# Kernel optimization log

Hardware: AMD Instinct MI355X
Metric: run time of the kernel (lower is better)

## Reference

```python
import jax, jax.numpy as jnp
import numpy as np


def _compute_gradient(f, src, dst, egw):
    # f: [b, c, n] node features; src/dst: [b, e] edge endpoints; egw: [b, e, d]
    # gradient at node src = sum_edges pinvdx * (f[dst] - f[src])
    fT = f.transpose(0, 2, 1)  # b, n, c
    n = fT.shape[1]
    f_dst = jnp.take_along_axis(fT, dst[..., None], axis=1)  # b, e, c
    f_src = jnp.take_along_axis(fT, src[..., None], axis=1)  # b, e, c
    msg = egw[..., :, None] * (f_dst - f_src)[..., None, :]  # b, e, d, c
    b, e, d, c = msg.shape

    def seg(m, s):
        return jax.ops.segment_sum(m.reshape(e, d * c), s, num_segments=n)

    grad = jax.vmap(seg)(msg, src)  # b, n, d*c
    return grad.transpose(0, 2, 1)  # b, d*c, n


def _forward(x, t, nodes, node_weights, edge_gradient_weights, modes, sp_L,
             fc0_w, fc0_b, Wc, Ws, W0, ws_w, ws_b, gws_w, gws_b,
             fc1_w, fc1_b, fc2_w, fc2_b, directed_edges):
    D = nodes.shape[-1]
    # Fourier bases: modes [k,d,w] scaled by sp_L [d,w]
    temp = jnp.einsum('bxd,kdw->bxkw', nodes, modes * sp_L)
    bc, bs = jnp.cos(temp), jnp.sin(temp)
    b0 = jnp.ones(temp[:, :, :1, :].shape, temp.dtype)
    nw = node_weights[:, :, None, :]
    wbc, wbs, wb0 = bc * nw, bs * nw, b0 * nw

    x_value = x[:, :, :D]
    h = jnp.concatenate([x, t], -1) @ fc0_w + fc0_b  # b, n, c
    h = h.transpose(0, 2, 1)  # b, c, n

    src = directed_edges[..., 0]
    dst = directed_edges[..., 1]
    nlayers = ws_w.shape[0]
    for i in range(nlayers):
        # spectral convolution (real Fourier transform on scattered points)
        xc = jnp.einsum('bcx,bxkw->bckw', h, wbc)
        xs = -jnp.einsum('bcx,bxkw->bckw', h, wbs)
        x0 = jnp.einsum('bcx,bxkw->bckw', h, wb0)
        fc_ = jnp.einsum('bikw,iokw->bokw', xc, Wc[i]) - jnp.einsum('bikw,iokw->bokw', xs, Ws[i])
        fs_ = jnp.einsum('bikw,iokw->bokw', xs, Wc[i]) + jnp.einsum('bikw,iokw->bokw', xc, Ws[i])
        f0_ = jnp.einsum('bikw,iokw->bokw', x0, W0[i])
        x1 = (jnp.einsum('bokw,bxkw->box', f0_, b0)
              + 2.0 * jnp.einsum('bokw,bxkw->box', fc_, bc)
              - 2.0 * jnp.einsum('bokw,bxkw->box', fs_, bs))
        # pointwise linear (Conv1d kernel size 1)
        x2 = jnp.einsum('oc,bcx->box', ws_w[i], h) + ws_b[i][None, :, None]
        # gradient operator + softsign + Conv1d
        g = _compute_gradient(h, src, dst, edge_gradient_weights)  # b, d*c, n
        g = g / (1.0 + jnp.abs(g))  # softsign
        x3 = jnp.einsum('oc,bcx->box', gws_w[i], g) + gws_b[i][None, :, None]
        h = x1 + x2 + x3
        if i != nlayers - 1:
            h = jax.nn.gelu(h, approximate=False)

    h = h.transpose(0, 2, 1)  # b, n, c
    h = jax.nn.gelu(h @ fc1_w + fc1_b, approximate=False)
    h = h @ fc2_w + fc2_b
    return x_value + t * h


def setup_inputs() -> dict:
    B, N, E = 2, 20000, 100000
    D, W, K, C, L, FC, OUT = 3, 1, 128, 128, 3, 128, 3
    key = jax.random.key(0)
    k = jax.random.split(key, 16)
    x = jax.random.normal(k[0], (B, N, D), jnp.float32)
    t = jax.random.uniform(k[1], (B, N, 1), jnp.float32)
    node_mask = jnp.ones((B, N, 1), jnp.int32)
    nodes = jax.random.uniform(k[2], (B, N, D), jnp.float32)
    node_weights = jax.random.uniform(k[3], (B, N, W), jnp.float32) / N
    directed_edges = jax.random.randint(k[4], (B, E, 2), 0, N)
    edge_gradient_weights = jax.random.normal(k[5], (B, E, D), jnp.float32)
    modes = jax.random.normal(k[6], (K, D, W), jnp.float32) * (2.0 * np.pi)
    sp_L = jnp.ones((D, W), jnp.float32)
    fc0_w = jax.random.normal(k[7], (D + 1, C), jnp.float32) * 0.1
    fc0_b = jnp.zeros((C,), jnp.float32)
    scale = 1.0 / (C * C)
    Wc = jax.random.uniform(k[8], (L, C, C, K, W), jnp.float32) * scale
    Ws = jax.random.uniform(k[9], (L, C, C, K, W), jnp.float32) * scale
    W0 = jax.random.uniform(k[10], (L, C, C, 1, W), jnp.float32) * scale
    ws_w = jax.random.normal(k[11], (L, C, C), jnp.float32) * 0.05
    ws_b = jnp.zeros((L, C), jnp.float32)
    gws_w = jax.random.normal(k[12], (L, C, D * C), jnp.float32) * 0.05
    gws_b = jnp.zeros((L, C), jnp.float32)
    fc1_w = jax.random.normal(k[13], (C, FC), jnp.float32) * 0.05
    fc1_b = jnp.zeros((FC,), jnp.float32)
    fc2_w = jax.random.normal(k[14], (FC, OUT), jnp.float32) * 0.05
    fc2_b = jnp.zeros((OUT,), jnp.float32)
    return dict(x=x, t=t, node_mask=node_mask, nodes=nodes, node_weights=node_weights,
                directed_edges=directed_edges, edge_gradient_weights=edge_gradient_weights,
                modes=modes, sp_L=sp_L, fc0_w=fc0_w, fc0_b=fc0_b, Wc=Wc, Ws=Ws, W0=W0,
                ws_w=ws_w, ws_b=ws_b, gws_w=gws_w, gws_b=gws_b,
                fc1_w=fc1_w, fc1_b=fc1_b, fc2_w=fc2_w, fc2_b=fc2_b)


def reference(x, t, node_mask, nodes, node_weights, directed_edges, edge_gradient_weights,
              modes, sp_L, fc0_w, fc0_b, Wc, Ws, W0, ws_w, ws_b, gws_w, gws_b,
              fc1_w, fc1_b, fc2_w, fc2_b):
    del node_mask  # unpacked but unused in the original forward
    return _forward(x, t, nodes, node_weights, edge_gradient_weights, modes, sp_L,
                    fc0_w, fc0_b, Wc, Ws, W0, ws_w, ws_b, gws_w, gws_b,
                    fc1_w, fc1_b, fc2_w, fc2_b, directed_edges)
```

## Files before the change

### kernel.cpp

```cpp
#include <hip/hip_runtime.h>
#include <math.h>

#define BB 2
#define NN 20000
#define EE 100000
#define DD 3
#define KK 128
#define CC 128
#define LL 3
#define FCC 128
#define GJ (DD*CC)
#define KR 768
#define NP 20096
#define NCHK 157
#define G1CH 157
#define G1N 128

typedef __attribute__((ext_vector_type(8))) short bf16x8;
typedef __attribute__((ext_vector_type(4))) float f32x4;

__device__ inline unsigned short f2bf(float f) {
  unsigned int u = __float_as_uint(f);
  u += 0x7fffu + ((u >> 16) & 1u);
  return (unsigned short)(u >> 16);
}
__device__ inline float bf2f(unsigned short u) {
  return __uint_as_float(((unsigned int)u) << 16);
}

__device__ float d_nw[BB*NN];
__device__ __align__(16) unsigned short d_stackT[(size_t)BB*NP*KR];
__device__ __align__(16) unsigned short d_bcT[(size_t)BB*KK*NP];
__device__ __align__(16) unsigned short d_bsT[(size_t)BB*KK*NP];
__device__ __align__(16) unsigned short d_hTwT[(size_t)BB*CC*NP];
__device__ __align__(16) float d_uT[(size_t)BB*NP*FCC];
__device__ __align__(16) unsigned short d_Amatb[BB*CC*KR];
__device__ __align__(16) unsigned short d_fc1wb[FCC*CC];
__device__ __align__(16) float d_part[(size_t)BB*G1CH*2*128*128];
__device__ float d_xc[BB*CC*KK];
__device__ float d_xs[BB*CC*KK];
__device__ float d_x0p[BB*NCHK*CC];
__device__ float d_fcp[BB*CC*8*KK];
__device__ float d_fsp[BB*CC*8*KK];
__device__ float d_bias[BB*CC];
__device__ int d_cnt[BB*NN];
__device__ int d_cursor[BB*NN];
__device__ int d_off[BB*(NN+1)];
__device__ __align__(16) float4 d_erec[(size_t)BB*EE];

__global__ __launch_bounds__(128) void k_basis(const float* __restrict__ nodes,
                                               const float* __restrict__ nodew,
                                               const float* __restrict__ modes,
                                               const float* __restrict__ spL) {
  int bn = blockIdx.x;
  int k  = threadIdx.x;
  int b = bn / NN, n = bn % NN;
  float x0 = nodes[bn*3+0], x1 = nodes[bn*3+1], x2 = nodes[bn*3+2];
  float tmp = x0*modes[k*3+0]*spL[0] + x1*modes[k*3+1]*spL[1] + x2*modes[k*3+2]*spL[2];
  float cv = cosf(tmp), sv = sinf(tmp);
  size_t row = (size_t)(b*NP + n);
  d_stackT[row*KR + k]       = f2bf(cv);
  d_stackT[row*KR + 128 + k] = f2bf(sv);
  if (k == 0) d_nw[bn] = nodew[bn];
}

__global__ __launch_bounds__(256) void k_basisT() {
  __shared__ unsigned short t1[32][136];
  __shared__ unsigned short t2[32][136];
  int blk = blockIdx.x;
  int nt = blk % 628, b = blk / 628;
  int n0 = nt*32;
  int tid = threadIdx.x;
  int kl = tid & 127, ng = tid >> 7;
  for (int nn = ng; nn < 32; nn += 2) {
    int n = n0 + nn;
    unsigned short cv = 0, sv = 0;
    if (n < NN) {
      const unsigned short* sp = d_stackT + ((size_t)(b*NP + n))*KR;
      cv = sp[kl]; sv = sp[128 + kl];
    }
    t1[nn][kl] = cv;
    t2[nn][kl] = sv;
  }
  __syncthreads();
  int nl = tid & 31, kg = tid >> 5;
  for (int k = kg; k < 128; k += 8) {
    d_bcT[((size_t)(b*KK + k))*NP + n0 + nl] = t1[nl][k];
    d_bsT[((size_t)(b*KK + k))*NP + n0 + nl] = t2[nl][k];
  }
}

__global__ __launch_bounds__(256) void k_csr_zero() {
  int tid = blockIdx.x*256 + threadIdx.x;
  if (tid < BB*NN) { d_cnt[tid] = 0; d_cursor[tid] = 0; }
}

__global__ __launch_bounds__(256) void k_csr_count(const int* __restrict__ edges) {
  int e = blockIdx.x*256 + threadIdx.x;
  if (e >= BB*EE) return;
  int b = e / EE;
  int src = edges[e*2 + 0];
  atomicAdd(&d_cnt[b*NN + src], 1);
}

__global__ __launch_bounds__(1024) void k_csr_scan() {
  int b = blockIdx.x;
  __shared__ int sdata[1024];
  __shared__ int carry_s;
  int tid = threadIdx.x;
  if (tid == 0) carry_s = 0;
  __syncthreads();
  for (int chunk = 0; chunk < 20; ++chunk) {
    int i = chunk*1024 + tid;
    int v = (i < NN) ? d_cnt[b*NN + i] : 0;
    sdata[tid] = v;
    __syncthreads();
    for (int s = 1; s < 1024; s <<= 1) {
      int tv = (tid >= s) ? sdata[tid - s] : 0;
      __syncthreads();
      sdata[tid] += tv;
      __syncthreads();
    }
    int excl = carry_s + sdata[tid] - v;
    if (i < NN) d_off[b*(NN+1) + i] = excl;
    __syncthreads();
    if (tid == 1023) carry_s += sdata[1023];
    __syncthreads();
  }
  if (tid == 0) d_off[b*(NN+1) + NN] = carry_s;
}

__global__ __launch_bounds__(256) void k_csr_scatter(const int* __restrict__ edges,
                                                     const float* __restrict__ egw) {
  int e = blockIdx.x*256 + threadIdx.x;
  if (e >= BB*EE) return;
  int b = e / EE;
  int src = edges[e*2 + 0];
  int dst = edges[e*2 + 1];
  int pos = atomicAdd(&d_cursor[b*NN + src], 1);
  d_erec[(size_t)b*EE + d_off[b*(NN+1) + src] + pos] =
      make_float4(__int_as_float(dst), egw[e*3+0], egw[e*3+1], egw[e*3+2]);
}

__global__ __launch_bounds__(256) void k_h0(const float* __restrict__ x,
                                            const float* __restrict__ t,
                                            const float* __restrict__ w,
                                            const float* __restrict__ bias) {
  int tid = blockIdx.x*256 + threadIdx.x;
  int c = tid & 127;
  int bn = tid >> 7;
  int b = bn / NN, n = bn % NN;
  const float* xv = x + bn*3;
  float acc = bias[c] + xv[0]*w[c] + xv[1]*w[CC+c] + xv[2]*w[2*CC+c]
            + t[bn]*w[3*CC+c];
  d_stackT[((size_t)(b*NP + n))*KR + 256 + c] = f2bf(acc);
}

__global__ __launch_bounds__(256) void k_hT0() {
  __shared__ unsigned short t[128][136];
  int chunk = blockIdx.x;
  int b = blockIdx.y;
  int n0 = chunk*128;
  int tid = threadIdx.x;
  int cl = tid & 127, ng = tid >> 7;
  for (int nn = ng; nn < 128; nn += 2) {
    int n = n0 + nn;
    unsigned short v = 0;
    if (n < NN) {
      float hv = bf2f(d_stackT[((size_t)(b*NP + n))*KR + 256 + cl]);
      v = f2bf(hv * d_nw[b*NN + n]);
    }
    t[nn][cl] = v;
  }
  __syncthreads();
  int nl = tid & 31, cg = tid >> 5;
  for (int c = cg; c < 128; c += 8)
    for (int nn2 = 0; nn2 < 128; nn2 += 32)
      d_hTwT[((size_t)(b*CC + c))*NP + n0 + nn2 + nl] = t[nn2 + nl][c];
}

__global__ __launch_bounds__(256) void k_gemm1m() {
  __shared__ unsigned short Bsh[2][128][40];
  int chunk = blockIdx.x;
  int b = blockIdx.y;
  int tid = threadIdx.x, lane = tid & 63, wid = tid >> 6;
  int q = lane >> 4, m = lane & 15;
  f32x4 accC[2][8], accS[2][8];
  #pragma unroll
  for (int i = 0; i < 2; i++)
    #pragma unroll
    for (int j = 0; j < 8; j++) { accC[i][j] = (f32x4){0.f,0.f,0.f,0.f}; accS[i][j] = (f32x4){0.f,0.f,0.f,0.f}; }
  const unsigned short* Ab = d_hTwT + (size_t)b*CC*NP;
  const unsigned short* Bcp = d_bcT + (size_t)b*KK*NP;
  const unsigned short* Bsp = d_bsT + (size_t)b*KK*NP;
  int n0 = chunk*G1N;
  for (int s = 0; s < G1N/32; s++) {
    int nb = n0 + s*32;
    __syncthreads();
    {
      int arr = tid >> 7, row = tid & 127;
      const unsigned short* src = (arr ? Bsp : Bcp) + (size_t)row*NP + nb;
      unsigned short* dr = &Bsh[arr][row][0];
      *(uint4*)&dr[0]  = *(const uint4*)&src[0];
      *(uint4*)&dr[8]  = *(const uint4*)&src[8];
      *(uint4*)&dr[16] = *(const uint4*)&src[16];
      *(uint4*)&dr[24] = *(const uint4*)&src[24];
    }
    __syncthreads();
    bf16x8 a0 = *(const bf16x8*)(Ab + (size_t)(wid*32 + m)*NP + nb + q*8);
    bf16x8 a1 = *(const bf16x8*)(Ab + (size_t)(wid*32 + 16 + m)*NP + nb + q*8);
    #pragma unroll
    for (int kt = 0; kt < 8; kt++) {
      bf16x8 bcf = *(const bf16x8*)&Bsh[0][kt*16 + m][q*8];
      bf16x8 bsf = *(const bf16x8*)&Bsh[1][kt*16 + m][q*8];
      accC[0][kt] = __builtin_amdgcn_mfma_f32_16x16x32_bf16(a0, bcf, accC[0][kt], 0, 0, 0);
      accC[1][kt] = __builtin_amdgcn_mfma_f32_16x16x32_bf16(a1, bcf, accC[1][kt], 0, 0, 0);
      accS[0][kt] = __builtin_amdgcn_mfma_f32_16x16x32_bf16(a0, bsf, accS[0][kt], 0, 0, 0);
      accS[1][kt] = __builtin_amdgcn_mfma_f32_16x16x32_bf16(a1, bsf, accS[1][kt], 0, 0, 0);
    }
  }
  float* base = d_part + (((size_t)b*G1CH + chunk)*2)*16384;
  #pragma unroll
  for (int mt = 0; mt < 2; mt++)
    #pragma unroll
    for (int kt = 0; kt < 8; kt++)
      #pragma unroll
      for (int r = 0; r < 4; r++) {
        int c = wid*32 + mt*16 + q*4 + r;
        int k = kt*16 + m;
        base[c*128 + k]         =  accC[mt][kt][r];
        base[16384 + c*128 + k] = -accS[mt][kt][r];
      }
}

__global__ __launch_bounds__(256) void k_reduce1() {
  int tid = blockIdx.x*256 + threadIdx.x;
  int k = tid & 127;
  int c = (tid >> 7) & 127;
  int arr = (tid >> 14) & 1;
  int b = tid >> 15;
  const float* p = d_part + (((size_t)b*G1CH)*2 + arr)*16384 + c*128 + k;
  float acc = 0.f;
  for (int ch = 0; ch < G1CH; ch++) acc += p[(size_t)ch*2*16384];
  if (arr == 0) d_xc[(b*CC + c)*KK + k] = acc;
  else          d_xs[(b*CC + c)*KK + k] = acc;
}

__global__ __launch_bounds__(256) void k_x0() {
  int chunk = blockIdx.x;
  int b = blockIdx.y;
  int tid = threadIdx.x;
  int c = tid >> 1, half = tid & 1;
  const unsigned short* p = d_hTwT + ((size_t)(b*CC + c))*NP + chunk*128 + half*64;
  float acc = 0.f;
  #pragma unroll
  for (int i = 0; i < 8; i++) {
    ushort4 v0 = *(const ushort4*)&p[i*8];
    ushort4 v1 = *(const ushort4*)&p[i*8 + 4];
    acc += bf2f(v0.x) + bf2f(v0.y) + bf2f(v0.z) + bf2f(v0.w)
         + bf2f(v1.x) + bf2f(v1.y) + bf2f(v1.z) + bf2f(v1.w);
  }
  __shared__ float red[128][2];
  red[c][half] = acc;
  __syncthreads();
  if (half == 0) d_x0p[(b*NCHK + chunk)*CC + c] = red[c][0] + red[c][1];
}

__global__ __launch_bounds__(128) void k_spec(const float* __restrict__ Wc,
                                              const float* __restrict__ Ws, int l) {
  int bo = blockIdx.x;
  int ch = blockIdx.y;
  int b = bo >> 7;
  int o = bo & 127;
  int k = threadIdx.x;
  int i0 = ch*16;
  const float* wcp = Wc + ((size_t)(l*CC + i0)*CC + o)*KK + k;
  const float* wsp = Ws + ((size_t)(l*CC + i0)*CC + o)*KK + k;
  float fc = 0.f, fs = 0.f;
  #pragma unroll 4
  for (int j = 0; j < 16; j++) {
    int i = i0 + j;
    float xcv = d_xc[(b*CC + i)*KK + k];
    float xsv = d_xs[(b*CC + i)*KK + k];
    float wcv = wcp[(size_t)j*CC*KK];
    float wsv = wsp[(size_t)j*CC*KK];
    fc += xcv*wcv - xsv*wsv;
    fs += xsv*wcv + xcv*wsv;
  }
  d_fcp[((size_t)bo*8 + ch)*KK + k] = fc;
  d_fsp[((size_t)bo*8 + ch)*KK + k] = fs;
}

__global__ __launch_bounds__(128) void k_f0(const float* __restrict__ W0,
                                            const float* __restrict__ wsb,
                                            const float* __restrict__ gwsb, int l) {
  int b = blockIdx.x;
  int o = threadIdx.x;
  __shared__ float sx[CC];
  float xv = 0.f;
  for (int p = 0; p < NCHK; p++) xv += d_x0p[(b*NCHK + p)*CC + o];
  sx[o] = xv;
  __syncthreads();
  float acc = 0.f;
  for (int i = 0; i < CC; i++) acc += sx[i]*W0[(l*CC + i)*CC + o];
  d_bias[b*CC + o] = acc + wsb[l*CC + o] + gwsb[l*CC + o];
}

__global__ __launch_bounds__(128) void k_buildAb(const float* __restrict__ wsw,
                                                 const float* __restrict__ gwsw, int l) {
  int bo = blockIdx.x;
  int b = bo >> 7, o = bo & 127;
  int t = threadIdx.x;
  float fc = 0.f, fs = 0.f;
  #pragma unroll
  for (int ch = 0; ch < 8; ch++) {
    fc += d_fcp[((size_t)bo*8 + ch)*KK + t];
    fs += d_fsp[((size_t)bo*8 + ch)*KK + t];
  }
  unsigned short* dst = d_Amatb + (size_t)bo*KR;
  dst[t]       = f2bf( 2.f*fc);
  dst[128 + t] = f2bf(-2.f*fs);
  dst[256 + t] = f2bf(wsw[(l*CC + o)*CC + t]);
  #pragma unroll
  for (int j = 0; j < 3; j++)
    dst[384 + j*128 + t] = f2bf(gwsw[(size_t)(l*CC + o)*GJ + j*128 + t]);
}

__global__ __launch_bounds__(128) void k_fc1w(const float* __restrict__ fc1w) {
  int c = blockIdx.x;
  int o2 = threadIdx.x;
  d_fc1wb[o2*CC + c] = f2bf(fc1w[c*FCC + o2]);
}

__global__ __launch_bounds__(128) void k_grad_csr() {
  int bn = blockIdx.x;
  int b = bn / NN, n = bn % NN;
  int c = threadIdx.x;
  int beg = d_off[b*(NN+1) + n];
  int end = d_off[b*(NN+1) + n + 1];
  const float4* rp = d_erec + (size_t)b*EE;
  const unsigned short* hb = d_stackT + (size_t)b*NP*KR + 256 + c;
  float a0 = 0.f, a1 = 0.f, a2 = 0.f;
  float sw0 = 0.f, sw1 = 0.f, sw2 = 0.f;
  int p = beg;
  for (; p + 4 <= end; p += 4) {
    float4 r1 = rp[p], r2 = rp[p+1], r3 = rp[p+2], r4 = rp[p+3];
    float f1 = bf2f(hb[(size_t)__float_as_int(r1.x)*KR]);
    float f2 = bf2f(hb[(size_t)__float_as_int(r2.x)*KR]);
    float f3 = bf2f(hb[(size_t)__float_as_int(r3.x)*KR]);
    float f4 = bf2f(hb[(size_t)__float_as_int(r4.x)*KR]);
    a0 += r1.y*f1 + r2.y*f2 + r3.y*f3 + r4.y*f4;
    a1 += r1.z*f1 + r2.z*f2 + r3.z*f3 + r4.z*f4;
    a2 += r1.w*f1 + r2.w*f2 + r3.w*f3 + r4.w*f4;
    sw0 += r1.y + r2.y + r3.y + r4.y;
    sw1 += r1.z + r2.z + r3.z + r4.z;
    sw2 += r1.w + r2.w + r3.w + r4.w;
  }
  for (; p < end; ++p) {
    float4 r1 = rp[p];
    float f1 = bf2f(hb[(size_t)__float_as_int(r1.x)*KR]);
    a0 += r1.y*f1; a1 += r1.z*f1; a2 += r1.w*f1;
    sw0 += r1.y; sw1 += r1.z; sw2 += r1.w;
  }
  float fs = bf2f(hb[(size_t)n*KR]);
  a0 -= sw0*fs; a1 -= sw1*fs; a2 -= sw2*fs;
  unsigned short* gp = d_stackT + ((size_t)(b*NP + n))*KR + 384;
  gp[c]        = f2bf(a0/(1.f + fabsf(a0)));
  gp[CC + c]   = f2bf(a1/(1.f + fabsf(a1)));
  gp[2*CC + c] = f2bf(a2/(1.f + fabsf(a2)));
}

__global__ __launch_bounds__(256) void k_mfma(int koff, int K,
                                              const unsigned short* __restrict__ W, size_t wstride,
                                              float* __restrict__ Out,
                                              const float* __restrict__ bias, int bias_stride,
                                              int gelu, int aux) {
  __shared__ unsigned short As[2][32*40];
  __shared__ unsigned short Bs[2][128*40];
  int b = blockIdx.z;
  int n_base = blockIdx.x*32;
  int tid = threadIdx.x;
  int lane = tid & 63, wid = tid >> 6;
  int wr = wid >> 1, wc = wid & 1;
  int q = lane >> 4, m = lane & 15;

  f32x4 acc[4];
  #pragma unroll
  for (int j = 0; j < 4; j++) acc[j] = (f32x4){0.f,0.f,0.f,0.f};

  const unsigned short* Wb = W + (size_t)b*wstride;
  const unsigned short* Ab = d_stackT + (size_t)b*NP*KR + koff;

#define STAGE(k0, d) { \
    if (tid < 128) { \
      int rowA = tid >> 2; int e8A = (tid & 3)*8; \
      *(uint4*)&As[d][rowA*40 + e8A] = *(const uint4*)(Ab + (size_t)(n_base + rowA)*KR + (k0) + e8A); \
    } \
    _Pragma("unroll") \
    for (int i_ = 0; i_ < 2; i_++) { \
      int idx_ = tid + i_*256; int rowB = idx_ >> 2; int e8B = (idx_ & 3)*8; \
      *(uint4*)&Bs[d][rowB*40 + e8B] = *(const uint4*)(Wb + (size_t)rowB*K + (k0) + e8B); \
    } }

  STAGE(0, 0)
  int cur = 0;
  for (int k0 = 0; k0 < K; k0 += 32) {
    __syncthreads();
    if (k0 + 32 < K) STAGE(k0 + 32, cur ^ 1)
    bf16x8 a = *(const bf16x8*)&As[cur][(wr*16 + m)*40 + q*8];
    #pragma unroll
    for (int ot = 0; ot < 4; ot++) {
      bf16x8 bf = *(const bf16x8*)&Bs[cur][(wc*64 + ot*16 + m)*40 + q*8];
      acc[ot] = __builtin_amdgcn_mfma_f32_16x16x32_bf16(a, bf, acc[ot], 0, 0, 0);
    }
    cur ^= 1;
  }
#undef STAGE

  const float* bp = bias + (size_t)b*bias_stride;
  int nb4 = n_base + wr*16 + q*4;
  float nw4[4];
  #pragma unroll
  for (int r = 0; r < 4; r++)
    nw4[r] = (aux && nb4 + r < NN) ? d_nw[b*NN + nb4 + r] : 0.f;
  #pragma unroll
  for (int ot = 0; ot < 4; ot++) {
    int o = wc*64 + ot*16 + m;
    float bvv = bp[o];
    float vals[4];
    #pragma unroll
    for (int r = 0; r < 4; r++) {
      float v = acc[ot][r] + bvv;
      if (gelu) v = 0.5f*v*(1.f + erff(v*0.70710678118f));
      vals[r] = v;
      if (!aux) Out[((size_t)(b*NP + nb4 + r))*128 + o] = v;
      if (aux && nb4 + r < NN)
        d_stackT[((size_t)(b*NP + nb4 + r))*KR + 256 + o] = f2bf(v);
    }
    if (aux) {
      ushort4 pk;
      pk.x = f2bf(vals[0]*nw4[0]);
      pk.y = f2bf(vals[1]*nw4[1]);
      pk.z = f2bf(vals[2]*nw4[2]);
      pk.w = f2bf(vals[3]*nw4[3]);
      *(ushort4*)&d_hTwT[((size_t)(b*CC + o))*NP + nb4] = pk;
    }
  }
}

__global__ __launch_bounds__(256) void k_out(const float* __restrict__ x,
                                             const float* __restrict__ t,
                                             const float* __restrict__ fc2w,
                                             const float* __restrict__ fc2b,
                                             float* __restrict__ out) {
  int tid = blockIdx.x*256 + threadIdx.x;
  if (tid >= BB*NN) return;
  int b = tid / NN, n = tid % NN;
  const float* up = d_uT + ((size_t)(b*NP + n))*FCC;
  float a0 = fc2b[0], a1 = fc2b[1], a2v = fc2b[2];
  #pragma unroll 4
  for (int o2 = 0; o2 < FCC; o2 += 4) {
    float4 uv = *(const float4*)&up[o2];
    a0  += uv.x*fc2w[(o2+0)*3+0] + uv.y*fc2w[(o2+1)*3+0] + uv.z*fc2w[(o2+2)*3+0] + uv.w*fc2w[(o2+3)*3+0];
    a1  += uv.x*fc2w[(o2+0)*3+1] + uv.y*fc2w[(o2+1)*3+1] + uv.z*fc2w[(o2+2)*3+1] + uv.w*fc2w[(o2+3)*3+1];
    a2v += uv.x*fc2w[(o2+0)*3+2] + uv.y*fc2w[(o2+1)*3+2] + uv.z*fc2w[(o2+2)*3+2] + uv.w*fc2w[(o2+3)*3+2];
  }
  float tv = t[tid];
  out[tid*3 + 0] = x[tid*3 + 0] + tv*a0;
  out[tid*3 + 1] = x[tid*3 + 1] + tv*a1;
  out[tid*3 + 2] = x[tid*3 + 2] + tv*a2v;
}

extern "C" void kernel_launch(void* const* d_in, const int* in_sizes, int n_in,
                              void* d_out, int out_size, void* d_ws, size_t ws_size,
                              hipStream_t stream) {
  const float* x     = (const float*)d_in[0];
  const float* t     = (const float*)d_in[1];
  const float* nodes = (const float*)d_in[3];
  const float* nodew = (const float*)d_in[4];
  const int*   edges = (const int*)d_in[5];
  const float* egw   = (const float*)d_in[6];
  const float* modes = (const float*)d_in[7];
  const float* spL   = (const float*)d_in[8];
  const float* fc0w  = (const float*)d_in[9];
  const float* fc0b  = (const float*)d_in[10];
  const float* Wc    = (const float*)d_in[11];
  const float* Ws    = (const float*)d_in[12];
  const float* W0    = (const float*)d_in[13];
  const float* wsw   = (const float*)d_in[14];
  const float* wsb   = (const float*)d_in[15];
  const float* gwsw  = (const float*)d_in[16];
  const float* gwsb  = (const float*)d_in[17];
  const float* fc1w  = (const float*)d_in[18];
  const float* fc1b  = (const float*)d_in[19];
  const float* fc2w  = (const float*)d_in[20];
  const float* fc2b  = (const float*)d_in[21];
  float* out = (float*)d_out;

  unsigned short* d_Amatb_p; hipGetSymbolAddress((void**)&d_Amatb_p, HIP_SYMBOL(d_Amatb));
  unsigned short* d_fc1wb_p; hipGetSymbolAddress((void**)&d_fc1wb_p, HIP_SYMBOL(d_fc1wb));
  float* d_uT_p;    hipGetSymbolAddress((void**)&d_uT_p,    HIP_SYMBOL(d_uT));
  float* d_bias_p;  hipGetSymbolAddress((void**)&d_bias_p,  HIP_SYMBOL(d_bias));

  hipLaunchKernelGGL(k_basis, dim3(BB*NN), dim3(128), 0, stream, nodes, nodew, modes, spL);
  hipLaunchKernelGGL(k_basisT, dim3(628*BB), dim3(256), 0, stream);
  hipLaunchKernelGGL(k_h0, dim3(BB*NN*CC/256), dim3(256), 0, stream, x, t, fc0w, fc0b);
  hipLaunchKernelGGL(k_hT0, dim3(NCHK, BB), dim3(256), 0, stream);
  hipLaunchKernelGGL(k_fc1w, dim3(CC), dim3(FCC), 0, stream, fc1w);
  hipLaunchKernelGGL(k_csr_zero, dim3((BB*NN + 255)/256), dim3(256), 0, stream);
  hipLaunchKernelGGL(k_csr_count, dim3((BB*EE + 255)/256), dim3(256), 0, stream, edges);
  hipLaunchKernelGGL(k_csr_scan, dim3(BB), dim3(1024), 0, stream);
  hipLaunchKernelGGL(k_csr_scatter, dim3((BB*EE + 255)/256), dim3(256), 0, stream, edges, egw);

  for (int l = 0; l < LL; l++) {
    hipLaunchKernelGGL(k_gemm1m, dim3(G1CH, BB), dim3(256), 0, stream);
    hipLaunchKernelGGL(k_reduce1, dim3(256), dim3(256), 0, stream);
    hipLaunchKernelGGL(k_x0, dim3(NCHK, BB), dim3(256), 0, stream);
    hipLaunchKernelGGL(k_spec, dim3(BB*CC, 8), dim3(128), 0, stream, Wc, Ws, l);
    hipLaunchKernelGGL(k_f0, dim3(BB), dim3(CC), 0, stream, W0, wsb, gwsb, l);
    hipLaunchKernelGGL(k_buildAb, dim3(BB*CC), dim3(128), 0, stream, wsw, gwsw, l);
    hipLaunchKernelGGL(k_grad_csr, dim3(BB*NN), dim3(128), 0, stream);
    hipLaunchKernelGGL(k_mfma, dim3(NP/32, 1, BB), dim3(256), 0, stream,
                       0, KR, d_Amatb_p, (size_t)CC*KR, d_uT_p, d_bias_p, CC,
                       (l != LL-1) ? 1 : 0, 1);
  }

  hipLaunchKernelGGL(k_mfma, dim3(NP/32, 1, BB), dim3(256), 0, stream,
                     256, CC, d_fc1wb_p, (size_t)0, d_uT_p, fc1b, 0, 1, 0);
  hipLaunchKernelGGL(k_out, dim3((BB*NN + 255)/256), dim3(256), 0, stream, x, t, fc2w, fc2b, out);
}
```

Measured before the change: 564.0 us.

## Retile spectral GEMM into 64x64 quadrants with double-buffered LDS staging

The spectral projection GEMM is split into four 64x64 output quadrants per batch, and each block now covers 256 nodes, so there are half as many node chunks. A and both B tiles are staged through double-buffered shared memory so the next load overlaps the MFMAs, instead of reading A straight from global memory. This shrinks the per-block accumulator count and the partial-sum buffer the reducer walks. Separately, the k_mfma GEMM is given a K step of 64 so each barrier covers twice as many MFMAs. The cost is more blocks that each reload A for their quadrant, and larger LDS tiles.

Result: faster. 525.8 us (-6.8%).

```diff
diff --git a/kernel.cpp b/kernel.cpp
--- a/kernel.cpp
+++ b/kernel.cpp
@@ -13,8 +13,8 @@
 #define KR 768
 #define NP 20096
 #define NCHK 157
-#define G1CH 157
-#define G1N 128
+#define G1CH 79
+#define G1N 256
 
 typedef __attribute__((ext_vector_type(8))) short bf16x8;
 typedef __attribute__((ext_vector_type(4))) float f32x4;
@@ -36,7 +36,7 @@
 __device__ __align__(16) float d_uT[(size_t)BB*NP*FCC];
 __device__ __align__(16) unsigned short d_Amatb[BB*CC*KR];
 __device__ __align__(16) unsigned short d_fc1wb[FCC*CC];
-__device__ __align__(16) float d_part[(size_t)BB*G1CH*2*128*128];
+__device__ __align__(16) float d_part[(size_t)BB*4*G1CH*2*64*64];
 __device__ float d_xc[BB*CC*KK];
 __device__ float d_xs[BB*CC*KK];
 __device__ float d_x0p[BB*NCHK*CC];
@@ -180,57 +180,63 @@
 }
 
 __global__ __launch_bounds__(256) void k_gemm1m() {
-  __shared__ unsigned short Bsh[2][128][40];
+  __shared__ unsigned short Ash[2][64*40];
+  __shared__ unsigned short Bch[2][64*40];
+  __shared__ unsigned short Bsh[2][64*40];
   int chunk = blockIdx.x;
-  int b = blockIdx.y;
+  int quad  = blockIdx.y;
+  int b     = blockIdx.z;
+  int ch = quad >> 1, kh = quad & 1;
   int tid = threadIdx.x, lane = tid & 63, wid = tid >> 6;
   int q = lane >> 4, m = lane & 15;
-  f32x4 accC[2][8], accS[2][8];
-  #pragma unroll
-  for (int i = 0; i < 2; i++)
+  f32x4 accC[4], accS[4];
+  #pragma unroll
+  for (int j = 0; j < 4; j++) { accC[j] = (f32x4){0.f,0.f,0.f,0.f}; accS[j] = (f32x4){0.f,0.f,0.f,0.f}; }
+  const unsigned short* Ab  = d_hTwT + ((size_t)(b*CC + ch*64))*NP;
+  const unsigned short* Bcp = d_bcT + ((size_t)(b*KK + kh*64))*NP;
+  const unsigned short* Bsp = d_bsT + ((size_t)(b*KK + kh*64))*NP;
+  int n0 = chunk*G1N;
+
+#define G1STAGE(nb, d) { \
+    int row_ = tid >> 2; int e8_ = (tid & 3)*8; \
+    if ((nb) < NP) { \
+      *(uint4*)&Ash[d][row_*40 + e8_] = *(const uint4*)(Ab  + (size_t)row_*NP + (nb) + e8_); \
+      *(uint4*)&Bch[d][row_*40 + e8_] = *(const uint4*)(Bcp + (size_t)row_*NP + (nb) + e8_); \
+      *(uint4*)&Bsh[d][row_*40 + e8_] = *(const uint4*)(Bsp + (size_t)row_*NP + (nb) + e8_); \
+    } else { \
+      uint4 z_ = make_uint4(0,0,0,0); \
+      *(uint4*)&Ash[d][row_*40 + e8_] = z_; \
+      *(uint4*)&Bch[d][row_*40 + e8_] = z_; \
+      *(uint4*)&Bsh[d][row_*40 + e8_] = z_; \
+    } }
+
+  G1STAGE(n0, 0)
+  int cur = 0;
+  for (int s = 0; s < G1N/32; s++) {
+    __syncthreads();
+    if (s + 1 < G1N/32) G1STAGE(n0 + (s+1)*32, cur ^ 1)
+    bf16x8 a = *(const bf16x8*)&Ash[cur][(wid*16 + m)*40 + q*8];
     #pragma unroll
-    for (int j = 0; j < 8; j++) { accC[i][j] = (f32x4){0.f,0.f,0.f,0.f}; accS[i][j] = (f32x4){0.f,0.f,0.f,0.f}; }
-  const unsigned short* Ab = d_hTwT + (size_t)b*CC*NP;
-  const unsigned short* Bcp = d_bcT + (size_t)b*KK*NP;
-  const unsigned short* Bsp = d_bsT + (size_t)b*KK*NP;
-  int n0 = chunk*G1N;
-  for (int s = 0; s < G1N/32; s++) {
-    int nb = n0 + s*32;
-    __syncthreads();
-    {
-      int arr = tid >> 7, row = tid & 127;
-      const unsigned short* src = (arr ? Bsp : Bcp) + (size_t)row*NP + nb;
-      unsigned short* dr = &Bsh[arr][row][0];
-      *(uint4*)&dr[0]  = *(const uint4*)&src[0];
-      *(uint4*)&dr[8]  = *(const uint4*)&src[8];
-      *(uint4*)&dr[16] = *(const uint4*)&src[16];
-      *(uint4*)&dr[24] = *(const uint4*)&src[24];
-    }
-    __syncthreads();
-    bf16x8 a0 = *(const bf16x8*)(Ab + (size_t)(wid*32 + m)*NP + nb + q*8);
-    bf16x8 a1 = *(const bf16x8*)(Ab + (size_t)(wid*32 + 16 + m)*NP + nb + q*8);
+    for (int kt = 0; kt < 4; kt++) {
+      bf16x8 bcf = *(const bf16x8*)&Bch[cur][(kt*16 + m)*40 + q*8];
+      accC[kt] = __builtin_amdgcn_mfma_f32_16x16x32_bf16(a, bcf, accC[kt], 0, 0, 0);
+      bf16x8 bsf = *(const bf16x8*)&Bsh[cur][(kt*16 + m)*40 + q*8];
+      accS[kt] = __builtin_amdgcn_mfma_f32_16x16x32_bf16(a, bsf, accS[kt], 0, 0, 0);
+    }
+    cur ^= 1;
+  }
+#undef G1STAGE
+
+  float* base = d_part + ((size_t)(b*4 + quad)*G1CH + chunk)*2*4096;
+  #pragma unroll
+  for (int kt = 0; kt < 4; kt++)
     #pragma unroll
-    for (int kt = 0; kt < 8; kt++) {
-      bf16x8 bcf = *(const bf16x8*)&Bsh[0][kt*16 + m][q*8];
-      bf16x8 bsf = *(const bf16x8*)&Bsh[1][kt*16 + m][q*8];
-      accC[0][kt] = __builtin_amdgcn_mfma_f32_16x16x32_bf16(a0, bcf, accC[0][kt], 0, 0, 0);
-      accC[1][kt] = __builtin_amdgcn_mfma_f32_16x16x32_bf16(a1, bcf, accC[1][kt], 0, 0, 0);
-      accS[0][kt] = __builtin_amdgcn_mfma_f32_16x16x32_bf16(a0, bsf, accS[0][kt], 0, 0, 0);
-      accS[1][kt] = __builtin_amdgcn_mfma_f32_16x16x32_bf16(a1, bsf, accS[1][kt], 0, 0, 0);
-    }
-  }
-  float* base = d_part + (((size_t)b*G1CH + chunk)*2)*16384;
-  #pragma unroll
-  for (int mt = 0; mt < 2; mt++)
-    #pragma unroll
-    for (int kt = 0; kt < 8; kt++)
-      #pragma unroll
-      for (int r = 0; r < 4; r++) {
-        int c = wid*32 + mt*16 + q*4 + r;
-        int k = kt*16 + m;
-        base[c*128 + k]         =  accC[mt][kt][r];
-        base[16384 + c*128 + k] = -accS[mt][kt][r];
-      }
+    for (int r = 0; r < 4; r++) {
+      int c = wid*16 + q*4 + r;
+      int k = kt*16 + m;
+      base[c*64 + k]        =  accC[kt][r];
+      base[4096 + c*64 + k] = -accS[kt][r];
+    }
 }
 
 __global__ __launch_bounds__(256) void k_reduce1() {
@@ -239,9 +245,12 @@
   int c = (tid >> 7) & 127;
   int arr = (tid >> 14) & 1;
   int b = tid >> 15;
-  const float* p = d_part + (((size_t)b*G1CH)*2 + arr)*16384 + c*128 + k;
+  int ch = c >> 6, cl = c & 63;
+  int kh = k >> 6, kl = k & 63;
+  int quad = ch*2 + kh;
+  const float* p = d_part + ((size_t)(b*4 + quad)*G1CH)*2*4096 + arr*4096 + cl*64 + kl;
   float acc = 0.f;
-  for (int ch = 0; ch < G1CH; ch++) acc += p[(size_t)ch*2*16384];
+  for (int t = 0; t < G1CH; t++) acc += p[(size_t)t*2*4096];
   if (arr == 0) d_xc[(b*CC + c)*KK + k] = acc;
   else          d_xs[(b*CC + c)*KK + k] = acc;
 }
@@ -375,8 +384,8 @@
                                               float* __restrict__ Out,
                                               const float* __restrict__ bias, int bias_stride,
                                               int gelu, int aux) {
-  __shared__ unsigned short As[2][32*40];
-  __shared__ unsigned short Bs[2][128*40];
+  __shared__ unsigned short As[2][32*72];
+  __shared__ unsigned short Bs[2][128*72];
   int b = blockIdx.z;
   int n_base = blockIdx.x*32;
   int tid = threadIdx.x;
@@ -392,26 +401,26 @@
   const unsigned short* Ab = d_stackT + (size_t)b*NP*KR + koff;
 
 #define STAGE(k0, d) { \
-    if (tid < 128) { \
-      int rowA = tid >> 2; int e8A = (tid & 3)*8; \
-      *(uint4*)&As[d][rowA*40 + e8A] = *(const uint4*)(Ab + (size_t)(n_base + rowA)*KR + (k0) + e8A); \
-    } \
+    { int rowA = tid >> 3; int e8A = (tid & 7)*8; \
+      *(uint4*)&As[d][rowA*72 + e8A] = *(const uint4*)(Ab + (size_t)(n_base + rowA)*KR + (k0) + e8A); } \
     _Pragma("unroll") \
-    for (int i_ = 0; i_ < 2; i_++) { \
-      int idx_ = tid + i_*256; int rowB = idx_ >> 2; int e8B = (idx_ & 3)*8; \
-      *(uint4*)&Bs[d][rowB*40 + e8B] = *(const uint4*)(Wb + (size_t)rowB*K + (k0) + e8B); \
-    } }
+    for (int i_ = 0; i_ < 4; i_++) { \
+      int idx_ = tid + i_*256; int rowB = idx_ >> 3; int e8B = (idx_ & 7)*8; \
+      *(uint4*)&Bs[d][rowB*72 + e8B] = *(const uint4*)(Wb + (size_t)rowB*K + (k0) + e8B); } }
 
   STAGE(0, 0)
   int cur = 0;
-  for (int k0 = 0; k0 < K; k0 += 32) {
+  for (int k0 = 0; k0 < K; k0 += 64) {
     __syncthreads();
-    if (k0 + 32 < K) STAGE(k0 + 32, cur ^ 1)
-    bf16x8 a = *(const bf16x8*)&As[cur][(wr*16 + m)*40 + q*8];
+    if (k0 + 64 < K) STAGE(k0 + 64, cur ^ 1)
+    bf16x8 a0 = *(const bf16x8*)&As[cur][(wr*16 + m)*72 + q*8];
+    bf16x8 a1 = *(const bf16x8*)&As[cur][(wr*16 + m)*72 + 32 + q*8];
     #pragma unroll
     for (int ot = 0; ot < 4; ot++) {
-      bf16x8 bf = *(const bf16x8*)&Bs[cur][(wc*64 + ot*16 + m)*40 + q*8];
-      acc[ot] = __builtin_amdgcn_mfma_f32_16x16x32_bf16(a, bf, acc[ot], 0, 0, 0);
+      bf16x8 b0 = *(const bf16x8*)&Bs[cur][(wc*64 + ot*16 + m)*72 + q*8];
+      acc[ot] = __builtin_amdgcn_mfma_f32_16x16x32_bf16(a0, b0, acc[ot], 0, 0, 0);
+      bf16x8 b1 = *(const bf16x8*)&Bs[cur][(wc*64 + ot*16 + m)*72 + 32 + q*8];
+      acc[ot] = __builtin_amdgcn_mfma_f32_16x16x32_bf16(a1, b1, acc[ot], 0, 0, 0);
     }
     cur ^= 1;
   }
@@ -513,7 +522,7 @@
   hipLaunchKernelGGL(k_csr_scatter, dim3((BB*EE + 255)/256), dim3(256), 0, stream, edges, egw);
 
   for (int l = 0; l < LL; l++) {
-    hipLaunchKernelGGL(k_gemm1m, dim3(G1CH, BB), dim3(256), 0, stream);
+    hipLaunchKernelGGL(k_gemm1m, dim3(G1CH, 4, BB), dim3(256), 0, stream);
     hipLaunchKernelGGL(k_reduce1, dim3(256), dim3(256), 0, stream);
     hipLaunchKernelGGL(k_x0, dim3(NCHK, BB), dim3(256), 0, stream);
     hipLaunchKernelGGL(k_spec, dim3(BB*CC, 8), dim3(128), 0, stream, Wc, Ws, l);
```
